# Kernel tuning notes

Measured on AMD Instinct MI355X. Metric: run time of the kernel, lower is better.

The kernel has to match this reference:

```python
import jax, jax.numpy as jnp
import numpy as np

B, T, C, H = 8, 2048, 768, 64

def setup_inputs() -> dict:
    key = jax.random.key(0)
    k1, k2, k3, k4 = jax.random.split(key, 4)
    x = jax.random.normal(k1, (B, T, C), dtype=jnp.float32)
    Wk = jax.random.normal(k2, (C, H), dtype=jnp.float32) * 0.02
    Wq = jax.random.normal(k3, (C, H), dtype=jnp.float32) * 0.02
    Wv = jax.random.normal(k4, (C, H), dtype=jnp.float32) * 0.02
    return {"x": x, "Wk": Wk, "Wq": Wq, "Wv": Wv}

def reference(x, Wk, Wq, Wv):
    # QKV projections (no bias): [B,T,C] @ [C,H] -> [B,T,H]
    k = jnp.einsum('btc,ch->bth', x, Wk)
    q = jnp.einsum('btc,ch->bth', x, Wq)
    v = jnp.einsum('btc,ch->bth', x, Wv)
    scale = 1.0 / jnp.sqrt(jnp.asarray(q.shape[-1], q.dtype))
    # scores: [B,T,T]
    wei = jnp.einsum('bth,bsh->bts', q, k) * scale
    # causal mask: upper triangle (k=1) set to -inf before softmax
    causal = jnp.tril(jnp.ones((wei.shape[1], wei.shape[2]), dtype=bool))
    wei = jnp.where(causal[None, :, :], wei, -jnp.inf)
    wei = jax.nn.softmax(wei, axis=-1)
    # dropout deterministic (training=False) -> identity
    out = jnp.einsum('bts,bsh->bth', wei, v)
    return out
```

## Files before the change

kernel.cpp:

```cpp
#include <hip/hip_runtime.h>
#include <hip/hip_bf16.h>
#include <stdint.h>

#define BB 8
#define TT 2048
#define CC 768
#define NTPB 72

typedef __bf16 bf16x8 __attribute__((ext_vector_type(8)));
typedef float f32x4 __attribute__((ext_vector_type(4)));
typedef float f32x16 __attribute__((ext_vector_type(16)));

__device__ inline __bf16 f2b(float f) {
    __hip_bfloat16 h = __float2bfloat16(f);
    return __builtin_bit_cast(__bf16, h);
}
__device__ inline ushort f2bits(float f) {
    __hip_bfloat16 h = __float2bfloat16(f);
    return __builtin_bit_cast(ushort, h);
}
__device__ inline uint32_t cvtpk(float lo, float hi) {
    uint32_t r;
    asm("v_cvt_pk_bf16_f32 %0, %1, %2" : "=v"(r) : "v"(lo), "v"(hi));
    return r;
}
__device__ inline void pswap(uint32_t& a, uint32_t& b) {
    asm volatile("v_permlane32_swap_b32 %0, %1" : "+v"(a), "+v"(b));
}

#define GLL16(gp, lp)                                                          \
    __builtin_amdgcn_global_load_lds(                                          \
        (const __attribute__((address_space(1))) unsigned int*)(gp),           \
        (__attribute__((address_space(3))) unsigned int*)(lp), 16, 0, 0)

__launch_bounds__(256)
__global__ void wt_kernel(const float* __restrict__ Wk, const float* __restrict__ Wq,
                          const float* __restrict__ Wv, ushort* __restrict__ WtF) {
    __shared__ float tile[64][65];
    int m  = blockIdx.x / 12;
    int c0 = (blockIdx.x % 12) * 64;
    const float* W = (m == 0) ? Wq : ((m == 1) ? Wk : Wv);
    int tid = threadIdx.x;
#pragma unroll
    for (int i = 0; i < 4; i++) {
        int r   = (tid >> 4) + i * 16;
        int col = (tid & 15) * 4;
        float4 v = *(const float4*)&W[(size_t)(c0 + r) * 64 + col];
        tile[r][col] = v.x; tile[r][col + 1] = v.y;
        tile[r][col + 2] = v.z; tile[r][col + 3] = v.w;
    }
    __syncthreads();
    int j  = tid >> 2;
    int cc = (tid & 3) * 16;
    ushort tmp[16];
#pragma unroll
    for (int e = 0; e < 16; e++) tmp[e] = f2bits(tile[cc + e][j]);
    int c  = m * 64 + j;
    int kb = c0 + cc;
    int kc = kb >> 5;
    int h4 = (kb >> 3) & 3;
    ushort* dst = &WtF[((size_t)kc * 192 + c) * 32 + h4 * 8];
    *(uint4*)(dst)     = *(uint4*)&tmp[0];
    *(uint4*)(dst + 8) = *(uint4*)&tmp[8];
}

__launch_bounds__(256, 2)
__global__ void qkv_kernel(const float* __restrict__ x, const ushort* __restrict__ WtF,
                           ushort* __restrict__ qws, ushort* __restrict__ kws,
                           ushort* __restrict__ vws) {
    __shared__ float xs[4][32 * 64];

    int tid  = threadIdx.x;
    int wid  = tid >> 6;
    int lane = tid & 63;
    int l15  = lane & 15;
    int hi4  = lane >> 4;
    int row0 = blockIdx.x * 32;

    int ch0 = tid,        r0s = ch0 >> 4, gc0 = (ch0 & 15) ^ (r0s & 7);
    int ch1 = tid + 256,  r1s = ch1 >> 4, gc1 = (ch1 & 15) ^ (r1s & 7);
    const float* gp0 = x + (size_t)(row0 + r0s) * CC + gc0 * 4;
    const float* gp1 = x + (size_t)(row0 + r1s) * CC + gc1 * 4;

    const ushort* wtp[3];
#pragma unroll
    for (int nt = 0; nt < 3; nt++)
        wtp[nt] = WtF + ((size_t)(wid * 48 + nt * 16 + l15) * 4 + hi4) * 8;

    f32x4 acc[2][3];
#pragma unroll
    for (int mm = 0; mm < 2; mm++)
#pragma unroll
        for (int nt = 0; nt < 3; nt++) acc[mm][nt] = (f32x4){0.f, 0.f, 0.f, 0.f};

    auto stage = [&](int t) {
        int buf = t & 3;
        GLL16(gp0 + t * 64, &xs[buf][ch0 * 4]);
        GLL16(gp1 + t * 64, &xs[buf][ch1 * 4]);
    };

    stage(0); stage(1); stage(2); stage(3);

#pragma unroll
    for (int t = 0; t < 12; t++) {
        if (t < 9)       asm volatile("s_waitcnt vmcnt(6)" ::: "memory");
        else if (t == 9) asm volatile("s_waitcnt vmcnt(4)" ::: "memory");
        else if (t == 10) asm volatile("s_waitcnt vmcnt(2)" ::: "memory");
        else             asm volatile("s_waitcnt vmcnt(0)" ::: "memory");
        __builtin_amdgcn_s_barrier();
        __builtin_amdgcn_sched_barrier(0);

        int buf = t & 3;
#pragma unroll
        for (int ks = 0; ks < 2; ks++) {
            int kc = 2 * t + ks;
            bf16x8 af[2];
#pragma unroll
            for (int mm = 0; mm < 2; mm++) {
                int row = mm * 16 + l15;
                int g   = ks * 8 + hi4 * 2;
                const float* base = &xs[buf][row * 64];
                float4 fa = *(const float4*)(base + (((g)     ^ (row & 7)) * 4));
                float4 fb = *(const float4*)(base + (((g + 1) ^ (row & 7)) * 4));
                uint32_t w0 = cvtpk(fa.x, fa.y), w1 = cvtpk(fa.z, fa.w);
                uint32_t w2 = cvtpk(fb.x, fb.y), w3 = cvtpk(fb.z, fb.w);
                uint4 u = {w0, w1, w2, w3};
                af[mm] = __builtin_bit_cast(bf16x8, u);
            }
#pragma unroll
            for (int nt = 0; nt < 3; nt++) {
                bf16x8 b = __builtin_bit_cast(bf16x8,
                    *(const uint4*)(wtp[nt] + (size_t)kc * 6144));
                acc[0][nt] = __builtin_amdgcn_mfma_f32_16x16x32_bf16(af[0], b, acc[0][nt], 0, 0, 0);
                acc[1][nt] = __builtin_amdgcn_mfma_f32_16x16x32_bf16(af[1], b, acc[1][nt], 0, 0, 0);
            }
        }
        __builtin_amdgcn_s_barrier();
        if (t + 4 < 12) stage(t + 4);
    }

    int bidx = row0 >> 11;
#pragma unroll
    for (int mm = 0; mm < 2; mm++) {
        int r0 = row0 + mm * 16 + 4 * hi4;
        int t0 = r0 & 2047;
#pragma unroll
        for (int nt = 0; nt < 3; nt++) {
            int c = wid * 48 + nt * 16 + l15;
            int m = c >> 6;
            int j = c & 63;
            if (m == 0) {
#pragma unroll
                for (int r = 0; r < 4; r++)
                    qws[(size_t)(r0 + r) * 64 + j] = f2bits(acc[mm][nt][r] * 0.125f);
            } else if (m == 1) {
#pragma unroll
                for (int r = 0; r < 4; r++)
                    kws[(size_t)(r0 + r) * 64 + j] = f2bits(acc[mm][nt][r]);
            } else {
                ushort4 pk;
                pk.x = f2bits(acc[mm][nt][0]);
                pk.y = f2bits(acc[mm][nt][1]);
                pk.z = f2bits(acc[mm][nt][2]);
                pk.w = f2bits(acc[mm][nt][3]);
                *(ushort4*)&vws[((size_t)bidx * 64 + j) * TT + t0] = pk;
            }
        }
    }
}

__launch_bounds__(256, 3)
__global__ void flash_kernel(const ushort* __restrict__ qg, const ushort* __restrict__ kg,
                             const ushort* __restrict__ vtg, float* __restrict__ out,
                             float* __restrict__ pO, float* __restrict__ pM,
                             float* __restrict__ pL) {
    __shared__ ushort Ks[3][64 * 64];
    __shared__ ushort Vs[3][64 * 64];

    int tid  = threadIdx.x;
    int wid  = tid >> 6;
    int lane = tid & 63;
    int l31  = lane & 31;
    int hi   = lane >> 5;

    int b  = blockIdx.x / NTPB;
    int tp = blockIdx.x - b * NTPB;
    int g  = 0;
    while (tp >= ((g + 2) * (g + 2)) >> 2) g++;
    int seg   = tp - (((g + 1) * (g + 1)) >> 2);
    int nseg  = (g + 2) >> 1;
    int Qb    = g * 128;
    int Q0w   = Qb + wid * 32;
    int s_beg = seg * 256;
    int s_end = (s_beg + 256 < Qb + 128) ? s_beg + 256 : Qb + 128;
    int nt    = (s_end - s_beg) >> 6;

    int rS  = tid >> 3;
    int gcS = (tid & 7) ^ (rS & 7);
    const ushort* kS = kg  + ((size_t)b * TT + rS) * 64 + gcS * 8;
    const ushort* vS = vtg + ((size_t)b * 64 + rS) * TT + gcS * 8;

    auto stage = [&](int tt) {
        int buf = tt % 3;
        int ss  = s_beg + tt * 64;
        const ushort* kA = kS + (size_t)ss * 64;
        const ushort* vA = vS + ss;
        GLL16(kA,            &Ks[buf][tid * 8]);
        GLL16(kA + 32 * 64,  &Ks[buf][(tid + 256) * 8]);
        GLL16(vA,            &Vs[buf][tid * 8]);
        GLL16(vA + 32 * TT,  &Vs[buf][(tid + 256) * 8]);
    };

    const ushort* qp = qg + ((size_t)b * TT + Q0w + l31) * 64 + hi * 8;
    bf16x8 qf[4];
#pragma unroll
    for (int c = 0; c < 4; c++)
        qf[c] = __builtin_bit_cast(bf16x8, *(const uint4*)(qp + c * 16));

    f32x16 o0 = (f32x16)(0.f), o1 = (f32x16)(0.f);
    float m  = -INFINITY;
    float lp = 0.f;

    stage(0);
    if (nt > 1) stage(1);

    for (int t = 0; t < nt; t++) {
        if (t < nt - 1) asm volatile("s_waitcnt vmcnt(4)" ::: "memory");
        else            asm volatile("s_waitcnt vmcnt(0)" ::: "memory");
        __builtin_amdgcn_s_barrier();
        __builtin_amdgcn_sched_barrier(0);
        if (t + 2 < nt) stage(t + 2);

        int s0 = s_beg + t * 64;
        if (s0 < Q0w + 32) {
            int buf = t % 3;
            bf16x8 kf[2][4];
#pragma unroll
            for (int tt = 0; tt < 2; tt++) {
                int rk = tt * 32 + l31;
                const ushort* base = &Ks[buf][rk * 64];
                int sw = rk & 7;
#pragma unroll
                for (int c = 0; c < 4; c++)
                    kf[tt][c] = __builtin_bit_cast(bf16x8,
                        *(const uint4*)(base + (((c * 2 + hi) ^ sw) * 8)));
            }

            f32x16 st0 = (f32x16)(0.f), st1 = (f32x16)(0.f);
            __builtin_amdgcn_s_setprio(1);
#pragma unroll
            for (int c = 0; c < 4; c++)
                st0 = __builtin_amdgcn_mfma_f32_32x32x16_bf16(kf[0][c], qf[c], st0, 0, 0, 0);
#pragma unroll
            for (int c = 0; c < 4; c++)
                st1 = __builtin_amdgcn_mfma_f32_32x32x16_bf16(kf[1][c], qf[c], st1, 0, 0, 0);
            __builtin_amdgcn_s_setprio(0);

            if (s0 + 63 > Q0w) {
                int th0 = Q0w + l31 - s0 - 4 * hi;
                int th1 = th0 - 32;
#pragma unroll
                for (int r = 0; r < 16; r++) {
                    int kvl = (r & 3) + 8 * (r >> 2);
                    if (kvl > th0) st0[r] = -INFINITY;
                    if (kvl > th1) st1[r] = -INFINITY;
                }
            }

            float lmax = -INFINITY;
#pragma unroll
            for (int r = 0; r < 16; r++) lmax = fmaxf(lmax, fmaxf(st0[r], st1[r]));
            float pmax = fmaxf(lmax, __shfl_xor(lmax, 32));
            if (__any(pmax > m + 8.f)) {
                float mn = fmaxf(m, pmax);
                float al = __expf(m - mn);
                lp *= al;
#pragma unroll
                for (int r = 0; r < 16; r++) { o0[r] *= al; o1[r] *= al; }
                m = mn;
            }
#pragma unroll
            for (int r = 0; r < 16; r++) {
                st0[r] = __expf(st0[r] - m); lp += st0[r];
                st1[r] = __expf(st1[r] - m); lp += st1[r];
            }

            bf16x8 pf[4];
            {
                uint32_t w0, w1, w2, w3;
                w0 = cvtpk(st0[0], st0[1]);  w1 = cvtpk(st0[2], st0[3]);
                w2 = cvtpk(st0[4], st0[5]);  w3 = cvtpk(st0[6], st0[7]);
                pswap(w0, w2); pswap(w1, w3);
                uint4 u0 = {w0, w1, w2, w3}; pf[0] = __builtin_bit_cast(bf16x8, u0);
                w0 = cvtpk(st0[8], st0[9]);  w1 = cvtpk(st0[10], st0[11]);
                w2 = cvtpk(st0[12], st0[13]); w3 = cvtpk(st0[14], st0[15]);
                pswap(w0, w2); pswap(w1, w3);
                uint4 u1 = {w0, w1, w2, w3}; pf[1] = __builtin_bit_cast(bf16x8, u1);
                w0 = cvtpk(st1[0], st1[1]);  w1 = cvtpk(st1[2], st1[3]);
                w2 = cvtpk(st1[4], st1[5]);  w3 = cvtpk(st1[6], st1[7]);
                pswap(w0, w2); pswap(w1, w3);
                uint4 u2 = {w0, w1, w2, w3}; pf[2] = __builtin_bit_cast(bf16x8, u2);
                w0 = cvtpk(st1[8], st1[9]);  w1 = cvtpk(st1[10], st1[11]);
                w2 = cvtpk(st1[12], st1[13]); w3 = cvtpk(st1[14], st1[15]);
                pswap(w0, w2); pswap(w1, w3);
                uint4 u3 = {w0, w1, w2, w3}; pf[3] = __builtin_bit_cast(bf16x8, u3);
            }

            bf16x8 vf[2][4];
#pragma unroll
            for (int ht = 0; ht < 2; ht++) {
                int rv = ht * 32 + l31;
                const ushort* base = &Vs[buf][rv * 64];
                int sw = rv & 7;
#pragma unroll
                for (int c = 0; c < 4; c++)
                    vf[ht][c] = __builtin_bit_cast(bf16x8,
                        *(const uint4*)(base + (((c * 2 + hi) ^ sw) * 8)));
            }

            __builtin_amdgcn_s_setprio(1);
#pragma unroll
            for (int c = 0; c < 4; c++)
                o0 = __builtin_amdgcn_mfma_f32_32x32x16_bf16(vf[0][c], pf[c], o0, 0, 0, 0);
#pragma unroll
            for (int c = 0; c < 4; c++)
                o1 = __builtin_amdgcn_mfma_f32_32x32x16_bf16(vf[1][c], pf[c], o1, 0, 0, 0);
            __builtin_amdgcn_s_setprio(0);
        }
    }

    float lsum = lp + __shfl_xor(lp, 32);

    if (nseg == 1) {
        float inv = 1.f / lsum;
        float* ob = out + ((size_t)b * TT + Q0w + l31) * 64;
#pragma unroll
        for (int gg = 0; gg < 4; gg++) {
            float4 v0 = {o0[4*gg] * inv, o0[4*gg+1] * inv, o0[4*gg+2] * inv, o0[4*gg+3] * inv};
            *(float4*)(ob + 8 * gg + 4 * hi) = v0;
            float4 v1 = {o1[4*gg] * inv, o1[4*gg+1] * inv, o1[4*gg+2] * inv, o1[4*gg+3] * inv};
            *(float4*)(ob + 32 + 8 * gg + 4 * hi) = v1;
        }
    } else {
        int tb = b * NTPB + tp;
        float* pb = pO + (size_t)tb * 8192 + (size_t)(wid * 32 + l31) * 64;
#pragma unroll
        for (int gg = 0; gg < 4; gg++) {
            float4 v0 = {o0[4*gg], o0[4*gg+1], o0[4*gg+2], o0[4*gg+3]};
            *(float4*)(pb + 8 * gg + 4 * hi) = v0;
            float4 v1 = {o1[4*gg], o1[4*gg+1], o1[4*gg+2], o1[4*gg+3]};
            *(float4*)(pb + 32 + 8 * gg + 4 * hi) = v1;
        }
        if (hi == 0) {
            pM[(size_t)tb * 128 + wid * 32 + l31] = m;
            pL[(size_t)tb * 128 + wid * 32 + l31] = lsum;
        }
    }
}

__launch_bounds__(256)
__global__ void merge_kernel(const float* __restrict__ pO, const float* __restrict__ pM,
                             const float* __restrict__ pL, float* __restrict__ out) {
    int b    = blockIdx.x / 14;
    int g    = 2 + (blockIdx.x % 14);
    int nseg = (g + 2) >> 1;
    int tbase = b * NTPB + (((g + 1) * (g + 1)) >> 2);

    int row = threadIdx.x >> 1;
    int hh  = (threadIdx.x & 1) * 32;

    float mstar = -INFINITY;
    for (int s = 0; s < nseg; s++)
        mstar = fmaxf(mstar, pM[(size_t)(tbase + s) * 128 + row]);

    float oa[32];
#pragma unroll
    for (int i = 0; i < 32; i++) oa[i] = 0.f;
    float la = 0.f;
    for (int s = 0; s < nseg; s++) {
        float w = __expf(pM[(size_t)(tbase + s) * 128 + row] - mstar);
        la += w * pL[(size_t)(tbase + s) * 128 + row];
        const float* pp = pO + (size_t)(tbase + s) * 8192 + (size_t)row * 64 + hh;
#pragma unroll
        for (int i = 0; i < 8; i++) {
            float4 v = *(const float4*)(pp + i * 4);
            oa[i*4]   += w * v.x; oa[i*4+1] += w * v.y;
            oa[i*4+2] += w * v.z; oa[i*4+3] += w * v.w;
        }
    }
    float inv = 1.f / la;
    float* ob = out + ((size_t)b * TT + g * 128 + row) * 64 + hh;
#pragma unroll
    for (int i = 0; i < 8; i++) {
        float4 v = {oa[i*4] * inv, oa[i*4+1] * inv, oa[i*4+2] * inv, oa[i*4+3] * inv};
        *(float4*)(ob + i * 4) = v;
    }
}

extern "C" void kernel_launch(void* const* d_in, const int* in_sizes, int n_in,
                              void* d_out, int out_size, void* d_ws, size_t ws_size,
                              hipStream_t stream) {
    const float* x  = (const float*)d_in[0];
    const float* Wk = (const float*)d_in[1];
    const float* Wq = (const float*)d_in[2];
    const float* Wv = (const float*)d_in[3];
    float* out = (float*)d_out;

    char* ws = (char*)d_ws;
    ushort* WtF = (ushort*)(ws);
    ushort* qws = (ushort*)(ws + 0x50000);
    ushort* kws = (ushort*)(ws + 0x250000);
    ushort* vws = (ushort*)(ws + 0x450000);
    float*  pO  = (float*)(ws + 0x650000);
    float*  pM  = (float*)(ws + 0x1850000);
    float*  pL  = (float*)(ws + 0x1898000);

    wt_kernel<<<36, 256, 0, stream>>>(Wk, Wq, Wv, WtF);
    qkv_kernel<<<(BB * TT) / 32, 256, 0, stream>>>(x, WtF, qws, kws, vws);
    flash_kernel<<<BB * NTPB, 256, 0, stream>>>(qws, kws, vws, out, pO, pM, pL);
    merge_kernel<<<BB * 14, 256, 0, stream>>>(pO, pM, pL, out);
}
```

Measured before the change: 57.25 us.

## Stage QKV weight tiles through LDS with async loads alongside activations

The QKV projection kernel now copies the bf16 weight chunk for each k-step into shared memory with async global-to-LDS loads, using an XOR swizzle, instead of having every wave read weights directly from global memory inside the MFMA loop. The K pipeline is reworked from 12 steps of 64 columns to 24 steps of 32, with a 4-deep buffer ring for both x and W and adjusted vmcnt waits. This is meant to take global weight-load latency off the MFMA critical path and overlap it with compute. In exchange it uses more LDS per block, which may lower occupancy, and doubles the number of barriers per tile.

```diff
diff --git a/kernel.cpp b/kernel.cpp
--- a/kernel.cpp
+++ b/kernel.cpp
@@ -68,7 +68,8 @@
 __global__ void qkv_kernel(const float* __restrict__ x, const ushort* __restrict__ WtF,
                            ushort* __restrict__ qws, ushort* __restrict__ kws,
                            ushort* __restrict__ vws) {
-    __shared__ float xs[4][32 * 64];
+    __shared__ float  xsA[4][32 * 32];
+    __shared__ ushort xsB[4][6144];
 
     int tid  = threadIdx.x;
     int wid  = tid >> 6;
@@ -77,15 +78,21 @@
     int hi4  = lane >> 4;
     int row0 = blockIdx.x * 32;
 
-    int ch0 = tid,        r0s = ch0 >> 4, gc0 = (ch0 & 15) ^ (r0s & 7);
-    int ch1 = tid + 256,  r1s = ch1 >> 4, gc1 = (ch1 & 15) ^ (r1s & 7);
-    const float* gp0 = x + (size_t)(row0 + r0s) * CC + gc0 * 4;
-    const float* gp1 = x + (size_t)(row0 + r1s) * CC + gc1 * 4;
-
-    const ushort* wtp[3];
-#pragma unroll
-    for (int nt = 0; nt < 3; nt++)
-        wtp[nt] = WtF + ((size_t)(wid * 48 + nt * 16 + l15) * 4 + hi4) * 8;
+    int rA  = tid >> 3;
+    int gcA = (tid & 7) ^ (rA & 7);
+    const float* gpA = x + (size_t)(row0 + rA) * CC + gcA * 4;
+
+    int PB0 = tid, PB1 = tid + 256, PB2 = tid + 512;
+    int LB0 = PB0 ^ ((PB0 >> 3) & 3);
+    int LB1 = PB1 ^ ((PB1 >> 3) & 3);
+    int LB2 = PB2 ^ ((PB2 >> 3) & 3);
+
+    int PrB[3];
+#pragma unroll
+    for (int nt = 0; nt < 3; nt++) {
+        int Lr = (wid * 48 + nt * 16 + l15) * 4 + hi4;
+        PrB[nt] = Lr ^ ((Lr >> 3) & 3);
+    }
 
     f32x4 acc[2][3];
 #pragma unroll
@@ -95,48 +102,45 @@
 
     auto stage = [&](int t) {
         int buf = t & 3;
-        GLL16(gp0 + t * 64, &xs[buf][ch0 * 4]);
-        GLL16(gp1 + t * 64, &xs[buf][ch1 * 4]);
+        GLL16(gpA + t * 32, &xsA[buf][(size_t)tid * 4]);
+        const ushort* bsrc = WtF + (size_t)t * 6144;
+        GLL16(bsrc + LB0 * 8, &xsB[buf][PB0 * 8]);
+        GLL16(bsrc + LB1 * 8, &xsB[buf][PB1 * 8]);
+        GLL16(bsrc + LB2 * 8, &xsB[buf][PB2 * 8]);
     };
 
     stage(0); stage(1); stage(2); stage(3);
 
 #pragma unroll
-    for (int t = 0; t < 12; t++) {
-        if (t < 9)       asm volatile("s_waitcnt vmcnt(6)" ::: "memory");
-        else if (t == 9) asm volatile("s_waitcnt vmcnt(4)" ::: "memory");
-        else if (t == 10) asm volatile("s_waitcnt vmcnt(2)" ::: "memory");
-        else             asm volatile("s_waitcnt vmcnt(0)" ::: "memory");
+    for (int t = 0; t < 24; t++) {
+        if (t <= 20)      asm volatile("s_waitcnt vmcnt(12)" ::: "memory");
+        else if (t == 21) asm volatile("s_waitcnt vmcnt(8)" ::: "memory");
+        else if (t == 22) asm volatile("s_waitcnt vmcnt(4)" ::: "memory");
+        else              asm volatile("s_waitcnt vmcnt(0)" ::: "memory");
         __builtin_amdgcn_s_barrier();
         __builtin_amdgcn_sched_barrier(0);
 
         int buf = t & 3;
-#pragma unroll
-        for (int ks = 0; ks < 2; ks++) {
-            int kc = 2 * t + ks;
-            bf16x8 af[2];
-#pragma unroll
-            for (int mm = 0; mm < 2; mm++) {
-                int row = mm * 16 + l15;
-                int g   = ks * 8 + hi4 * 2;
-                const float* base = &xs[buf][row * 64];
-                float4 fa = *(const float4*)(base + (((g)     ^ (row & 7)) * 4));
-                float4 fb = *(const float4*)(base + (((g + 1) ^ (row & 7)) * 4));
-                uint32_t w0 = cvtpk(fa.x, fa.y), w1 = cvtpk(fa.z, fa.w);
-                uint32_t w2 = cvtpk(fb.x, fb.y), w3 = cvtpk(fb.z, fb.w);
-                uint4 u = {w0, w1, w2, w3};
-                af[mm] = __builtin_bit_cast(bf16x8, u);
-            }
-#pragma unroll
-            for (int nt = 0; nt < 3; nt++) {
-                bf16x8 b = __builtin_bit_cast(bf16x8,
-                    *(const uint4*)(wtp[nt] + (size_t)kc * 6144));
-                acc[0][nt] = __builtin_amdgcn_mfma_f32_16x16x32_bf16(af[0], b, acc[0][nt], 0, 0, 0);
-                acc[1][nt] = __builtin_amdgcn_mfma_f32_16x16x32_bf16(af[1], b, acc[1][nt], 0, 0, 0);
-            }
+        bf16x8 af[2];
+#pragma unroll
+        for (int mm = 0; mm < 2; mm++) {
+            int row = mm * 16 + l15;
+            const float* base = &xsA[buf][row * 32];
+            float4 fa = *(const float4*)(base + (((2 * hi4)     ^ (row & 7)) * 4));
+            float4 fb = *(const float4*)(base + (((2 * hi4 + 1) ^ (row & 7)) * 4));
+            uint32_t w0 = cvtpk(fa.x, fa.y), w1 = cvtpk(fa.z, fa.w);
+            uint32_t w2 = cvtpk(fb.x, fb.y), w3 = cvtpk(fb.z, fb.w);
+            uint4 u = {w0, w1, w2, w3};
+            af[mm] = __builtin_bit_cast(bf16x8, u);
+        }
+#pragma unroll
+        for (int nt = 0; nt < 3; nt++) {
+            bf16x8 b = __builtin_bit_cast(bf16x8, *(const uint4*)&xsB[buf][PrB[nt] * 8]);
+            acc[0][nt] = __builtin_amdgcn_mfma_f32_16x16x32_bf16(af[0], b, acc[0][nt], 0, 0, 0);
+            acc[1][nt] = __builtin_amdgcn_mfma_f32_16x16x32_bf16(af[1], b, acc[1][nt], 0, 0, 0);
         }
         __builtin_amdgcn_s_barrier();
-        if (t + 4 < 12) stage(t + 4);
+        if (t + 4 < 24) stage(t + 4);
     }
 
     int bidx = row0 >> 11;
```

Result: faster. 55.01 us (-3.9%).
